# Optimization experiments

Measured on AMD Instinct MI355X. Metric: run time of the kernel, lower is better.

Reference implementation:

```python
import jax, jax.numpy as jnp
import numpy as np

N_USER, N_PHOTO = 100_000, 200_000   # node counts per ntype
E = 1_000_000                        # edges per canonical etype
IN, OUT = 256, 64                    # in_size / out_size from HeteroRGCN defaults


def setup_inputs() -> dict:
    key = jax.random.key(0)
    ks = jax.random.split(key, 8)
    s = 1.0 / np.sqrt(IN)  # nn.Linear default init scale
    return {
        "user_feats": jax.random.normal(ks[0], (N_USER, IN), jnp.float32),   # learned self.user_feats
        "photo_feats": jax.random.normal(ks[1], (N_PHOTO, IN), jnp.float32),  # G.nodes['photo'].data['features']
        "W_likes": jax.random.uniform(ks[2], (IN, OUT), jnp.float32, -s, s),
        "b_likes": jnp.zeros((OUT,), jnp.float32),
        "W_likedby": jax.random.uniform(ks[3], (IN, OUT), jnp.float32, -s, s),
        "b_likedby": jnp.zeros((OUT,), jnp.float32),
        "likes_src": jax.random.randint(ks[4], (E,), 0, N_USER, jnp.int32),
        "likes_dst": jax.random.randint(ks[5], (E,), 0, N_PHOTO, jnp.int32),
        "likedby_src": jax.random.randint(ks[6], (E,), 0, N_PHOTO, jnp.int32),
        "likedby_dst": jax.random.randint(ks[7], (E,), 0, N_USER, jnp.int32),
    }


def _mean_agg(Wh_src, src, dst, n_dst):
    # DGL fn.copy_u + fn.mean: gather projected src feats along edges,
    # segment-sum into dst nodes, divide by in-degree (0-degree -> 0).
    msgs = Wh_src[src]  # [E, OUT] irregular gather
    tot = jax.ops.segment_sum(msgs, dst, num_segments=n_dst)
    deg = jax.ops.segment_sum(jnp.ones((src.shape[0],), msgs.dtype), dst, num_segments=n_dst)
    return tot / jnp.maximum(deg, 1.0)[:, None]


def reference(user_feats, photo_feats, W_likes, b_likes, W_likedby, b_likedby,
              likes_src, likes_dst, likedby_src, likedby_dst):
    # per-etype linear projection (self.weight[etype])
    Wh_likes = user_feats @ W_likes + b_likes        # src ntype 'user'
    Wh_likedby = photo_feats @ W_likedby + b_likedby  # src ntype 'photo'
    # multi_update_all({etype: (copy_u, mean)}, 'sum'); each dst ntype has one etype here
    h_photo = _mean_agg(Wh_likes, likes_src, likes_dst, N_PHOTO)
    h_user = _mean_agg(Wh_likedby, likedby_src, likedby_dst, N_USER)
    return h_user, h_photo
```

## Files before the change

### kernel.cpp

```cpp
#include <hip/hip_runtime.h>
#include <hip/hip_bf16.h>

#define N_USER 100000
#define N_PHOTO 200000
#define NEDGE 1000000
#define INF 256
#define OUTF 64

typedef unsigned short u16;
typedef __attribute__((ext_vector_type(8))) short short8;
typedef __attribute__((ext_vector_type(4))) short short4x;
typedef __attribute__((ext_vector_type(4))) float f32x4;

#define LDSPAD 264

#define BP 1563
#define BU 782
#define NB (BP + BU)
#define NE4 250000
#define TOT4 (2 * NE4)
#define CAP 8192

__device__ inline u16 f2b(float f) {
    union { float f; unsigned u; } v; v.f = f;
    unsigned r = v.u + 0x7FFF + ((v.u >> 16) & 1);
    return (u16)(r >> 16);
}
__device__ inline float b2f(u16 h) {
    union { unsigned u; float f; } v; v.u = ((unsigned)h) << 16; return v.f;
}

__global__ __launch_bounds__(256) void prep0(const float* __restrict__ W_likes,
                                             const float* __restrict__ W_likedby,
                                             u16* __restrict__ Wt_likes,
                                             u16* __restrict__ Wt_likedby,
                                             int* __restrict__ bucket_cnt) {
    int i = blockIdx.x * 256 + threadIdx.x;
    if (i < INF * OUTF) {
        int n = i & (OUTF - 1), k = i >> 6;
        Wt_likes[n * INF + k]   = f2b(W_likes[i]);
        Wt_likedby[n * INF + k] = f2b(W_likedby[i]);
    }
    if (i < NB) bucket_cnt[i] = 0;
}

__global__ __launch_bounds__(256) void proj_both(
    const float* __restrict__ user_feats, const float* __restrict__ photo_feats,
    const u16* __restrict__ Wt_likes, const u16* __restrict__ Wt_likedby,
    const float* __restrict__ b_likes, const float* __restrict__ b_likedby,
    u16* __restrict__ Wh_likes, u16* __restrict__ Wh_likedby)
{
    __shared__ u16 lds_wt[OUTF * LDSPAD];
    __shared__ u16 lds_a[64 * LDSPAD];
    const int NB_USER_PROJ = (N_USER + 63) / 64;
    int bb = blockIdx.x;
    const float* feats; const u16* Wt; const float* bias; u16* Wh; int nrows; int blk;
    if (bb < NB_USER_PROJ) { feats = user_feats;  Wt = Wt_likes;   bias = b_likes;   Wh = Wh_likes;   nrows = N_USER;  blk = bb; }
    else                   { feats = photo_feats; Wt = Wt_likedby; bias = b_likedby; Wh = Wh_likedby; nrows = N_PHOTO; blk = bb - NB_USER_PROJ; }

    int tid = threadIdx.x;
    for (int c = tid; c < (INF * OUTF) / 8; c += 256) {
        int n = c >> 5;
        int ko = (c & 31) * 8;
        *(short8*)&lds_wt[n * LDSPAD + ko] = *(const short8*)&Wt[n * INF + ko];
    }

    int r0 = blk * 64;
    #pragma unroll
    for (int it = 0; it < 16; ++it) {
        int idx = it * 256 + tid;
        int r = idx >> 6;
        int c4 = idx & 63;
        int row = r0 + r;
        float4 x = {0.f, 0.f, 0.f, 0.f};
        if (row < nrows) x = ((const float4*)(feats + (size_t)row * INF))[c4];
        short4x h = { (short)f2b(x.x), (short)f2b(x.y), (short)f2b(x.z), (short)f2b(x.w) };
        *(short4x*)&lds_a[r * LDSPAD + c4 * 4] = h;
    }
    __syncthreads();

    int wave = tid >> 6, lane = tid & 63;
    int l15 = lane & 15, quad = lane >> 4;

    f32x4 acc[4] = {{0,0,0,0},{0,0,0,0},{0,0,0,0},{0,0,0,0}};

    #pragma unroll
    for (int ks = 0; ks < 8; ++ks) {
        short8 a = *(const short8*)&lds_a[(wave * 16 + l15) * LDSPAD + ks * 32 + quad * 8];
        #pragma unroll
        for (int nt2 = 0; nt2 < 4; ++nt2) {
            short8 b = *(const short8*)&lds_wt[(nt2 * 16 + l15) * LDSPAD + ks * 32 + quad * 8];
            acc[nt2] = __builtin_amdgcn_mfma_f32_16x16x32_bf16(a, b, acc[nt2], 0, 0, 0);
        }
    }

    int rw0 = r0 + wave * 16;
    #pragma unroll
    for (int nt2 = 0; nt2 < 4; ++nt2) {
        int col = nt2 * 16 + l15;
        float bv = bias[col];
        #pragma unroll
        for (int r = 0; r < 4; ++r) {
            int row = rw0 + quad * 4 + r;
            if (row < nrows) {
                Wh[(size_t)row * OUTF + col] = f2b(acc[nt2][r] + bv);
            }
        }
    }
}

__global__ __launch_bounds__(256) void p1_hist(const int* __restrict__ likes_dst,
                                               const int* __restrict__ likedby_dst,
                                               int* __restrict__ bucket_cnt) {
    __shared__ int h[NB];
    int tid = threadIdx.x;
    for (int i = tid; i < NB; i += 256) h[i] = 0;
    __syncthreads();
    int gt = blockIdx.x * 256 + tid, nt = gridDim.x * 256;
    for (int i = gt; i < TOT4; i += nt) {
        bool L = i < NE4;
        int j = L ? i : i - NE4;
        int4 d = L ? ((const int4*)likes_dst)[j] : ((const int4*)likedby_dst)[j];
        int ofs = L ? 0 : BP;
        atomicAdd(&h[ofs + (d.x >> 7)], 1);
        atomicAdd(&h[ofs + (d.y >> 7)], 1);
        atomicAdd(&h[ofs + (d.z >> 7)], 1);
        atomicAdd(&h[ofs + (d.w >> 7)], 1);
    }
    __syncthreads();
    for (int i = tid; i < NB; i += 256) {
        int c = h[i];
        if (c) atomicAdd(&bucket_cnt[i], c);
    }
}

__global__ __launch_bounds__(256) void p2_scan(const int* __restrict__ bucket_cnt,
                                               int* __restrict__ bucket_off,
                                               int* __restrict__ bucket_cur) {
    __shared__ int lds[256];
    int t = threadIdx.x;
    int base_i = t * 10;
    int loc[10];
    int s = 0;
    #pragma unroll
    for (int k = 0; k < 10; ++k) {
        int idx = base_i + k;
        int v = (idx < NB) ? bucket_cnt[idx] : 0;
        loc[k] = s; s += v;
    }
    lds[t] = s;
    __syncthreads();
    for (int ofs = 1; ofs < 256; ofs <<= 1) {
        int v = (t >= ofs) ? lds[t - ofs] : 0;
        __syncthreads();
        lds[t] += v;
        __syncthreads();
    }
    int excl = lds[t] - s;
    #pragma unroll
    for (int k = 0; k < 10; ++k) {
        int idx = base_i + k;
        if (idx < NB) {
            int o = excl + loc[k];
            bucket_off[idx] = o;
            bucket_cur[idx] = o;
        }
    }
    if (t == 255) bucket_off[NB] = lds[255];
}

__global__ __launch_bounds__(256) void p3_part(
    const int* __restrict__ likes_src, const int* __restrict__ likes_dst,
    const int* __restrict__ likedby_src, const int* __restrict__ likedby_dst,
    int* __restrict__ bucket_cur, unsigned* __restrict__ part) {
    __shared__ int h[NB];
    int tid = threadIdx.x;
    for (int i = tid; i < NB; i += 256) h[i] = 0;
    __syncthreads();
    int gt = blockIdx.x * 256 + tid, nt = gridDim.x * 256;
    for (int i = gt; i < TOT4; i += nt) {
        bool L = i < NE4;
        int j = L ? i : i - NE4;
        int4 d = L ? ((const int4*)likes_dst)[j] : ((const int4*)likedby_dst)[j];
        int ofs = L ? 0 : BP;
        atomicAdd(&h[ofs + (d.x >> 7)], 1);
        atomicAdd(&h[ofs + (d.y >> 7)], 1);
        atomicAdd(&h[ofs + (d.z >> 7)], 1);
        atomicAdd(&h[ofs + (d.w >> 7)], 1);
    }
    __syncthreads();
    for (int i = tid; i < NB; i += 256) {
        int c = h[i];
        h[i] = c ? atomicAdd(&bucket_cur[i], c) : 0;
    }
    __syncthreads();
    for (int i = gt; i < TOT4; i += nt) {
        bool L = i < NE4;
        int j = L ? i : i - NE4;
        int4 d = L ? ((const int4*)likes_dst)[j] : ((const int4*)likedby_dst)[j];
        int4 s = L ? ((const int4*)likes_src)[j] : ((const int4*)likedby_src)[j];
        int ofs = L ? 0 : BP;
        int p;
        p = atomicAdd(&h[ofs + (d.x >> 7)], 1); part[p] = ((unsigned)s.x << 7) | (unsigned)(d.x & 127);
        p = atomicAdd(&h[ofs + (d.y >> 7)], 1); part[p] = ((unsigned)s.y << 7) | (unsigned)(d.y & 127);
        p = atomicAdd(&h[ofs + (d.z >> 7)], 1); part[p] = ((unsigned)s.z << 7) | (unsigned)(d.z & 127);
        p = atomicAdd(&h[ofs + (d.w >> 7)], 1); part[p] = ((unsigned)s.w << 7) | (unsigned)(d.w & 127);
    }
}

__global__ __launch_bounds__(256) void p4_reduce(
    const u16* __restrict__ Wh_likes, const u16* __restrict__ Wh_likedby,
    const int* __restrict__ bucket_off, const unsigned* __restrict__ part,
    float* __restrict__ out)
{
    __shared__ unsigned srt[CAP];
    __shared__ int hist[128];
    __shared__ int scn[129];
    __shared__ int cur[128];
    int b = blockIdx.x, t = threadIdx.x;
    const u16* Wh; float* obase; int node0, nn;
    if (b < BP) {
        Wh = Wh_likes; node0 = b << 7;
        nn = (node0 + 128 <= N_PHOTO) ? 128 : (N_PHOTO - node0);
        obase = out + ((size_t)N_USER + node0) * OUTF;
    } else {
        Wh = Wh_likedby; node0 = (b - BP) << 7;
        nn = (node0 + 128 <= N_USER) ? 128 : (N_USER - node0);
        obase = out + (size_t)node0 * OUTF;
    }
    int e0 = bucket_off[b], e1 = bucket_off[b + 1];
    int cnt = e1 - e0;

    if (cnt <= CAP) {
        if (t < 128) hist[t] = 0;
        __syncthreads();
        for (int e = e0 + t; e < e1; e += 256)
            atomicAdd(&hist[part[e] & 127], 1);
        __syncthreads();
        if (t == 0) scn[0] = 0;
        if (t < 128) scn[t + 1] = hist[t];
        __syncthreads();
        for (int ofs = 1; ofs < 128; ofs <<= 1) {
            int idx = t + 1;
            int v = (t < 128 && idx > ofs) ? scn[idx - ofs] : 0;
            __syncthreads();
            if (t < 128) scn[idx] += v;
            __syncthreads();
        }
        if (t < 128) cur[t] = scn[t];
        __syncthreads();
        for (int e = e0 + t; e < e1; e += 256) {
            unsigned v = part[e];
            int pos = atomicAdd(&cur[v & 127], 1);
            srt[pos] = v >> 7;
        }
        __syncthreads();

        int g = t >> 3, sub = t & 7;
        for (int dl = g; dl < 128; dl += 32) {
            int o0 = scn[dl], o1 = scn[dl + 1];
            f32x4 a0 = {0,0,0,0}, a1 = {0,0,0,0};
            int j = o0;
            for (; j + 4 <= o1; j += 4) {
                int s0 = srt[j], s1 = srt[j + 1], s2 = srt[j + 2], s3 = srt[j + 3];
                short8 v0 = *(const short8*)(Wh + (size_t)s0 * OUTF + sub * 8);
                short8 v1 = *(const short8*)(Wh + (size_t)s1 * OUTF + sub * 8);
                short8 v2 = *(const short8*)(Wh + (size_t)s2 * OUTF + sub * 8);
                short8 v3 = *(const short8*)(Wh + (size_t)s3 * OUTF + sub * 8);
                #pragma unroll
                for (int k = 0; k < 4; ++k) {
                    a0[k] += b2f((u16)v0[k]) + b2f((u16)v1[k]) + b2f((u16)v2[k]) + b2f((u16)v3[k]);
                    a1[k] += b2f((u16)v0[k + 4]) + b2f((u16)v1[k + 4]) + b2f((u16)v2[k + 4]) + b2f((u16)v3[k + 4]);
                }
            }
            for (; j < o1; ++j) {
                int s = srt[j];
                short8 v = *(const short8*)(Wh + (size_t)s * OUTF + sub * 8);
                #pragma unroll
                for (int k = 0; k < 4; ++k) {
                    a0[k] += b2f((u16)v[k]);
                    a1[k] += b2f((u16)v[k + 4]);
                }
            }
            int dgi = o1 - o0;
            float inv = 1.0f / (float)(dgi > 1 ? dgi : 1);
            if (dl < nn) {
                float* orow = obase + (size_t)dl * OUTF + sub * 8;
                float4 w0 = { a0[0] * inv, a0[1] * inv, a0[2] * inv, a0[3] * inv };
                float4 w1 = { a1[0] * inv, a1[1] * inv, a1[2] * inv, a1[3] * inv };
                *(float4*)orow = w0;
                *(float4*)(orow + 4) = w1;
            }
        }
    } else {
        float* acc = (float*)srt;
        for (int i = t; i < 128 * OUTF; i += 256) acc[i] = 0.f;
        if (t < 128) hist[t] = 0;
        __syncthreads();
        int hw = t >> 5, l = t & 31;
        for (int e = e0 + hw; e < e1; e += 8) {
            unsigned v = part[e];
            int src = (int)(v >> 7), dl = (int)(v & 127);
            unsigned w = ((const unsigned*)(Wh + (size_t)src * OUTF))[l];
            atomicAdd(&acc[dl * OUTF + 2 * l], b2f((u16)(w & 0xffff)));
            atomicAdd(&acc[dl * OUTF + 2 * l + 1], b2f((u16)(w >> 16)));
            if (l == 0) atomicAdd(&hist[dl], 1);
        }
        __syncthreads();
        for (int i = t; i < nn * (OUTF / 4); i += 256) {
            int node = i >> 4;
            int dg = hist[node];
            float inv = 1.0f / (float)(dg > 1 ? dg : 1);
            float4 vv = *(const float4*)&acc[node * OUTF + (i & 15) * 4];
            vv.x *= inv; vv.y *= inv; vv.z *= inv; vv.w *= inv;
            ((float4*)obase)[i] = vv;
        }
    }
}

extern "C" void kernel_launch(void* const* d_in, const int* in_sizes, int n_in,
                              void* d_out, int out_size, void* d_ws, size_t ws_size,
                              hipStream_t stream) {
    const float* user_feats  = (const float*)d_in[0];
    const float* photo_feats = (const float*)d_in[1];
    const float* W_likes     = (const float*)d_in[2];
    const float* b_likes     = (const float*)d_in[3];
    const float* W_likedby   = (const float*)d_in[4];
    const float* b_likedby   = (const float*)d_in[5];
    const int* likes_src     = (const int*)d_in[6];
    const int* likes_dst     = (const int*)d_in[7];
    const int* likedby_src   = (const int*)d_in[8];
    const int* likedby_dst   = (const int*)d_in[9];

    char* ws = (char*)d_ws;
    u16* Wh_likes     = (u16*)(ws + 0);
    u16* Wh_likedby   = (u16*)(ws + 12800000);
    u16* Wt_likes     = (u16*)(ws + 38400000);
    u16* Wt_likedby   = (u16*)(ws + 38432768);
    int* bucket_cnt   = (int*)(ws + 38465536);
    int* bucket_off   = (int*)(ws + 38474928);
    int* bucket_cur   = (int*)(ws + 38484320);
    unsigned* part    = (unsigned*)(ws + 38493712);

    float* out = (float*)d_out;

    prep0<<<64, 256, 0, stream>>>(W_likes, W_likedby, Wt_likes, Wt_likedby, bucket_cnt);

    proj_both<<<(N_USER + 63) / 64 + (N_PHOTO + 63) / 64, 256, 0, stream>>>(
        user_feats, photo_feats, Wt_likes, Wt_likedby, b_likes, b_likedby,
        Wh_likes, Wh_likedby);

    p1_hist<<<128, 256, 0, stream>>>(likes_dst, likedby_dst, bucket_cnt);

    p2_scan<<<1, 256, 0, stream>>>(bucket_cnt, bucket_off, bucket_cur);

    p3_part<<<128, 256, 0, stream>>>(likes_src, likes_dst, likedby_src, likedby_dst,
                                     bucket_cur, part);

    p4_reduce<<<NB, 256, 0, stream>>>(Wh_likes, Wh_likedby, bucket_off, part, out);
}
```

Before: 567.8 us.

## Merge histogram into projection kernel and stream A operand directly from global

Fuses the destination-bucket histogram kernel into the projection launch as extra blocks, removing one launch and letting the histogram overlap the GEMM. The projection no longer stages the activation tile in LDS. Each lane loads its fp32 row slice directly from global, converts it to bf16 in registers and feeds the MFMA. The weight tile in LDS switches from padding to an XOR swizzle, cutting LDS to 32KB, which may raise occupancy but makes global loads less coalesced.

```diff
diff --git a/kernel.cpp b/kernel.cpp
--- a/kernel.cpp
+++ b/kernel.cpp
@@ -9,10 +9,7 @@
 
 typedef unsigned short u16;
 typedef __attribute__((ext_vector_type(8))) short short8;
-typedef __attribute__((ext_vector_type(4))) short short4x;
 typedef __attribute__((ext_vector_type(4))) float f32x4;
-
-#define LDSPAD 264
 
 #define BP 1563
 #define BU 782
@@ -20,6 +17,11 @@
 #define NE4 250000
 #define TOT4 (2 * NE4)
 #define CAP 8192
+
+#define NPROJ_U ((N_USER + 63) / 64)
+#define NPROJ_P ((N_PHOTO + 63) / 64)
+#define NPROJ (NPROJ_U + NPROJ_P)
+#define NHIST 128
 
 __device__ inline u16 f2b(float f) {
     union { float f; unsigned u; } v; v.f = f;
@@ -44,93 +46,90 @@
     if (i < NB) bucket_cnt[i] = 0;
 }
 
-__global__ __launch_bounds__(256) void proj_both(
+__global__ __launch_bounds__(256) void work1(
     const float* __restrict__ user_feats, const float* __restrict__ photo_feats,
     const u16* __restrict__ Wt_likes, const u16* __restrict__ Wt_likedby,
     const float* __restrict__ b_likes, const float* __restrict__ b_likedby,
-    u16* __restrict__ Wh_likes, u16* __restrict__ Wh_likedby)
+    u16* __restrict__ Wh_likes, u16* __restrict__ Wh_likedby,
+    const int* __restrict__ likes_dst, const int* __restrict__ likedby_dst,
+    int* __restrict__ bucket_cnt)
 {
-    __shared__ u16 lds_wt[OUTF * LDSPAD];
-    __shared__ u16 lds_a[64 * LDSPAD];
-    const int NB_USER_PROJ = (N_USER + 63) / 64;
+    __shared__ __align__(16) char smem_raw[OUTF * 256 * 2];
     int bb = blockIdx.x;
+    int tid = threadIdx.x;
+
+    if (bb >= NPROJ) {
+        int* h = (int*)smem_raw;
+        for (int i = tid; i < NB; i += 256) h[i] = 0;
+        __syncthreads();
+        int hb = bb - NPROJ;
+        int gt = hb * 256 + tid, nt = NHIST * 256;
+        for (int i = gt; i < TOT4; i += nt) {
+            bool L = i < NE4;
+            int j = L ? i : i - NE4;
+            int4 d = L ? ((const int4*)likes_dst)[j] : ((const int4*)likedby_dst)[j];
+            int ofs = L ? 0 : BP;
+            atomicAdd(&h[ofs + (d.x >> 7)], 1);
+            atomicAdd(&h[ofs + (d.y >> 7)], 1);
+            atomicAdd(&h[ofs + (d.z >> 7)], 1);
+            atomicAdd(&h[ofs + (d.w >> 7)], 1);
+        }
+        __syncthreads();
+        for (int i = tid; i < NB; i += 256) {
+            int c = h[i];
+            if (c) atomicAdd(&bucket_cnt[i], c);
+        }
+        return;
+    }
+
+    u16* lds_wt = (u16*)smem_raw;
     const float* feats; const u16* Wt; const float* bias; u16* Wh; int nrows; int blk;
-    if (bb < NB_USER_PROJ) { feats = user_feats;  Wt = Wt_likes;   bias = b_likes;   Wh = Wh_likes;   nrows = N_USER;  blk = bb; }
-    else                   { feats = photo_feats; Wt = Wt_likedby; bias = b_likedby; Wh = Wh_likedby; nrows = N_PHOTO; blk = bb - NB_USER_PROJ; }
-
-    int tid = threadIdx.x;
+    if (bb < NPROJ_U) { feats = user_feats;  Wt = Wt_likes;   bias = b_likes;   Wh = Wh_likes;   nrows = N_USER;  blk = bb; }
+    else              { feats = photo_feats; Wt = Wt_likedby; bias = b_likedby; Wh = Wh_likedby; nrows = N_PHOTO; blk = bb - NPROJ_U; }
+
     for (int c = tid; c < (INF * OUTF) / 8; c += 256) {
         int n = c >> 5;
-        int ko = (c & 31) * 8;
-        *(short8*)&lds_wt[n * LDSPAD + ko] = *(const short8*)&Wt[n * INF + ko];
-    }
-
-    int r0 = blk * 64;
-    #pragma unroll
-    for (int it = 0; it < 16; ++it) {
-        int idx = it * 256 + tid;
-        int r = idx >> 6;
-        int c4 = idx & 63;
-        int row = r0 + r;
-        float4 x = {0.f, 0.f, 0.f, 0.f};
-        if (row < nrows) x = ((const float4*)(feats + (size_t)row * INF))[c4];
-        short4x h = { (short)f2b(x.x), (short)f2b(x.y), (short)f2b(x.z), (short)f2b(x.w) };
-        *(short4x*)&lds_a[r * LDSPAD + c4 * 4] = h;
+        int ko8 = c & 31;
+        int sw = ko8 ^ (n & 7);
+        *(short8*)&lds_wt[n * 256 + sw * 8] = *(const short8*)&Wt[n * INF + ko8 * 8];
     }
     __syncthreads();
 
     int wave = tid >> 6, lane = tid & 63;
     int l15 = lane & 15, quad = lane >> 4;
+    int r0 = blk * 64 + wave * 16;
+    int arow = r0 + l15;
+    bool arow_ok = arow < nrows;
 
     f32x4 acc[4] = {{0,0,0,0},{0,0,0,0},{0,0,0,0},{0,0,0,0}};
+    const float4* ap = (const float4*)(feats + (size_t)(arow_ok ? arow : 0) * INF);
 
     #pragma unroll
     for (int ks = 0; ks < 8; ++ks) {
-        short8 a = *(const short8*)&lds_a[(wave * 16 + l15) * LDSPAD + ks * 32 + quad * 8];
+        float4 x = ap[ks * 8 + quad * 2 + 0];
+        float4 y = ap[ks * 8 + quad * 2 + 1];
+        short8 a = { (short)f2b(x.x), (short)f2b(x.y), (short)f2b(x.z), (short)f2b(x.w),
+                     (short)f2b(y.x), (short)f2b(y.y), (short)f2b(y.z), (short)f2b(y.w) };
         #pragma unroll
         for (int nt2 = 0; nt2 < 4; ++nt2) {
-            short8 b = *(const short8*)&lds_wt[(nt2 * 16 + l15) * LDSPAD + ks * 32 + quad * 8];
+            int row = nt2 * 16 + l15;
+            int sw = (ks * 4 + quad) ^ (l15 & 7);
+            short8 b = *(const short8*)&lds_wt[row * 256 + sw * 8];
             acc[nt2] = __builtin_amdgcn_mfma_f32_16x16x32_bf16(a, b, acc[nt2], 0, 0, 0);
         }
     }
 
-    int rw0 = r0 + wave * 16;
     #pragma unroll
     for (int nt2 = 0; nt2 < 4; ++nt2) {
         int col = nt2 * 16 + l15;
         float bv = bias[col];
         #pragma unroll
         for (int r = 0; r < 4; ++r) {
-            int row = rw0 + quad * 4 + r;
+            int row = r0 + quad * 4 + r;
             if (row < nrows) {
                 Wh[(size_t)row * OUTF + col] = f2b(acc[nt2][r] + bv);
             }
         }
-    }
-}
-
-__global__ __launch_bounds__(256) void p1_hist(const int* __restrict__ likes_dst,
-                                               const int* __restrict__ likedby_dst,
-                                               int* __restrict__ bucket_cnt) {
-    __shared__ int h[NB];
-    int tid = threadIdx.x;
-    for (int i = tid; i < NB; i += 256) h[i] = 0;
-    __syncthreads();
-    int gt = blockIdx.x * 256 + tid, nt = gridDim.x * 256;
-    for (int i = gt; i < TOT4; i += nt) {
-        bool L = i < NE4;
-        int j = L ? i : i - NE4;
-        int4 d = L ? ((const int4*)likes_dst)[j] : ((const int4*)likedby_dst)[j];
-        int ofs = L ? 0 : BP;
-        atomicAdd(&h[ofs + (d.x >> 7)], 1);
-        atomicAdd(&h[ofs + (d.y >> 7)], 1);
-        atomicAdd(&h[ofs + (d.z >> 7)], 1);
-        atomicAdd(&h[ofs + (d.w >> 7)], 1);
-    }
-    __syncthreads();
-    for (int i = tid; i < NB; i += 256) {
-        int c = h[i];
-        if (c) atomicAdd(&bucket_cnt[i], c);
     }
 }
 
@@ -346,11 +345,9 @@
 
     prep0<<<64, 256, 0, stream>>>(W_likes, W_likedby, Wt_likes, Wt_likedby, bucket_cnt);
 
-    proj_both<<<(N_USER + 63) / 64 + (N_PHOTO + 63) / 64, 256, 0, stream>>>(
+    work1<<<NPROJ + NHIST, 256, 0, stream>>>(
         user_feats, photo_feats, Wt_likes, Wt_likedby, b_likes, b_likedby,
-        Wh_likes, Wh_likedby);
-
-    p1_hist<<<128, 256, 0, stream>>>(likes_dst, likedby_dst, bucket_cnt);
+        Wh_likes, Wh_likedby, likes_dst, likedby_dst, bucket_cnt);
 
     p2_scan<<<1, 256, 0, stream>>>(bucket_cnt, bucket_off, bucket_cur);
 
```

Result: faster. 496.1 us (-12.6%).
